# Performance work log

Measured on AMD Instinct MI355X. Metric: run time of the kernel, lower is better.

Reference implementation:

```python
import jax, jax.numpy as jnp
import numpy as np

INPUT_SIZE = 256
HIDDEN_SIZE = 512


def setup_inputs() -> dict:
    key = jax.random.key(0)
    ks = jax.random.split(key, 14)
    B, L, I, H = 64, 1024, INPUT_SIZE, HIDDEN_SIZE
    s = (1.0 / H) ** 0.5
    u = lambda k, shape: jax.random.uniform(k, shape, jnp.float32, -s, s)
    return {
        "inputs": jax.random.normal(ks[0], (B, L, I), jnp.float32),
        "hidden_states": jnp.zeros((1, B, H), jnp.float32),
        "w_ir": u(ks[1], (H, I)), "w_iz": u(ks[2], (H, I)), "w_in": u(ks[3], (H, I)),
        "b_ir": u(ks[4], (H,)), "b_iz": u(ks[5], (H,)), "b_in": u(ks[6], (H,)),
        "w_hr": u(ks[7], (H, H)), "w_hz": u(ks[8], (H, H)), "w_hn": u(ks[9], (H, H)),
        "b_hr": u(ks[10], (H,)), "b_hz": u(ks[11], (H,)), "b_hn": u(ks[12], (H,)),
    }


def _gru(inputs, h0, w_ir, w_iz, w_in, b_ir, b_iz, b_in,
         w_hr, w_hz, w_hn, b_hr, b_hz, b_hn):
    # Precompute all input projections in one big GEMM each (same math as per-step).
    # shapes: inputs [B,L,I] -> [B,L,H]
    xr = jnp.einsum("bli,hi->blh", inputs, w_ir) + b_ir
    xz = jnp.einsum("bli,hi->blh", inputs, w_iz) + b_iz
    xn = jnp.einsum("bli,hi->blh", inputs, w_in) + b_in

    def step(h, xt):
        xr_t, xz_t, xn_t = xt  # each [B,H]
        r = jax.nn.sigmoid(xr_t + h @ w_hr.T + b_hr)
        z = jax.nn.sigmoid(xz_t + h @ w_hz.T + b_hz)
        n = jnp.tanh(xn_t + r * (h @ w_hn.T + b_hn))
        h_new = (1.0 - z) * n + z * h
        return h_new, h_new

    # scan over time: move L to leading axis
    xs = (xr.transpose(1, 0, 2), xz.transpose(1, 0, 2), xn.transpose(1, 0, 2))
    h_last, hs = jax.lax.scan(step, h0[0], xs)  # hs: [L,B,H]
    outputs = hs.transpose(1, 0, 2)  # [B,L,H]
    return outputs, h_last[None]  # final hidden kept as (1,B,H) like the torch module


def reference(inputs, hidden_states, w_ir, w_iz, w_in, b_ir, b_iz, b_in,
              w_hr, w_hz, w_hn, b_hr, b_hz, b_hn):
    return _gru(inputs, hidden_states, w_ir, w_iz, w_in, b_ir, b_iz, b_in,
                w_hr, w_hz, w_hn, b_hr, b_hz, b_hn)
```

## Files before the change

kernel.cpp:

```cpp
#include <hip/hip_runtime.h>
#include <hip/hip_bf16.h>

typedef __attribute__((ext_vector_type(8))) short bf16x8;
typedef __attribute__((ext_vector_type(4))) float f32x4;


__device__ __forceinline__ unsigned short f2bf(float f) {
    __hip_bfloat16 h = __float2bfloat16(f);
    return __builtin_bit_cast(unsigned short, h);
}
__device__ __forceinline__ float bf2f(unsigned short u) {
    union { unsigned int i; float f; } c; c.i = ((unsigned int)u) << 16; return c.f;
}

__device__ __forceinline__ void store_h64(unsigned long long* p, unsigned long long v) {
    asm volatile("global_store_dwordx2 %0, %1, off sc0 sc1" :: "v"(p), "v"(v) : "memory");
}
__device__ __forceinline__ void store_flag(unsigned int* p, unsigned int v) {
    asm volatile("global_store_dword %0, %1, off sc0 sc1" :: "v"(p), "v"(v) : "memory");
}
__device__ __forceinline__ void vmem_drain() {
    asm volatile("s_waitcnt vmcnt(0)" ::: "memory");
}
__device__ __forceinline__ void lds_drain() {
    asm volatile("s_waitcnt lgkmcnt(0)" ::: "memory");
}

__global__ void pack_inputs(const float* __restrict__ in, unsigned short* __restrict__ out) {
    int i = blockIdx.x * 256 + threadIdx.x;
    float4 v = reinterpret_cast<const float4*>(in)[i];
    ushort4 u;
    u.x = f2bf(v.x); u.y = f2bf(v.y); u.z = f2bf(v.z); u.w = f2bf(v.w);
    reinterpret_cast<ushort4*>(out)[i] = u;
}

__global__ void pack_weights(const float* __restrict__ w_ir, const float* __restrict__ w_iz,
                             const float* __restrict__ w_in, const float* __restrict__ b_ir,
                             const float* __restrict__ b_iz, const float* __restrict__ b_in,
                             const float* __restrict__ w_hr, const float* __restrict__ w_hz,
                             const float* __restrict__ w_hn, const float* __restrict__ b_hr,
                             const float* __restrict__ b_hz,
                             unsigned short* __restrict__ Wx, unsigned short* __restrict__ Wh,
                             float* __restrict__ biasx, unsigned int* __restrict__ flags) {
    int i = blockIdx.x * 256 + threadIdx.x;
    {
        int g = i / 262144, rem = i % 262144;
        const float* src = (g == 0) ? w_hr : ((g == 1) ? w_hz : w_hn);
        Wh[i] = f2bf(src[rem]);
    }
    if (i < 393216) {
        int g = i / 131072, rem = i % 131072;
        const float* src = (g == 0) ? w_ir : ((g == 1) ? w_iz : w_in);
        Wx[i] = f2bf(src[rem]);
    }
    if (i < 1536) {
        int g = i / 512, j = i % 512;
        float v = (g == 0) ? (b_ir[j] + b_hr[j]) : ((g == 1) ? (b_iz[j] + b_hz[j]) : b_in[j]);
        biasx[i] = v;
    }
    if (i < 4096) flags[i] = 0u;
}

__global__ __launch_bounds__(256) void xproj_gemm(
    const unsigned short* __restrict__ A,
    const unsigned short* __restrict__ Bw,
    const float* __restrict__ biasx,
    unsigned short* __restrict__ X)
{
    __shared__ __attribute__((aligned(16))) unsigned short Al[64][40];
    __shared__ __attribute__((aligned(16))) unsigned short Bl[64][40];
    const int tid  = threadIdx.x;
    const int m0   = blockIdx.x * 64;
    const int n0   = blockIdx.y * 64;
    const int lane = tid & 63;
    const int wv   = tid >> 6;
    const int quad = lane >> 4;
    const int l16  = lane & 15;
    const int mw   = (wv & 1) * 32;
    const int nw   = (wv >> 1) * 32;
    const int lr   = tid >> 2;
    const int lc   = (tid & 3) * 8;

    f32x4 acc[2][2] = {};

    for (int kb = 0; kb < 8; ++kb) {
        uint4 av = *reinterpret_cast<const uint4*>(A  + (size_t)(m0 + lr) * 256 + kb * 32 + lc);
        uint4 bv = *reinterpret_cast<const uint4*>(Bw + (size_t)(n0 + lr) * 256 + kb * 32 + lc);
        __syncthreads();
        *reinterpret_cast<uint4*>(&Al[lr][lc]) = av;
        *reinterpret_cast<uint4*>(&Bl[lr][lc]) = bv;
        __syncthreads();
        bf16x8 af[2], bfg[2];
#pragma unroll
        for (int s = 0; s < 2; ++s) {
            af[s]  = *reinterpret_cast<const bf16x8*>(&Al[mw + s * 16 + l16][quad * 8]);
            bfg[s] = *reinterpret_cast<const bf16x8*>(&Bl[nw + s * 16 + l16][quad * 8]);
        }
#pragma unroll
        for (int sm = 0; sm < 2; ++sm)
#pragma unroll
            for (int sn = 0; sn < 2; ++sn)
                acc[sm][sn] = __builtin_amdgcn_mfma_f32_16x16x32_bf16(af[sm], bfg[sn], acc[sm][sn], 0, 0, 0);
    }
#pragma unroll
    for (int sn = 0; sn < 2; ++sn) {
        int n = n0 + nw + sn * 16 + l16;
        float bias = biasx[n];
#pragma unroll
        for (int sm = 0; sm < 2; ++sm)
#pragma unroll
            for (int r = 0; r < 4; ++r) {
                int m = m0 + mw + sm * 16 + quad * 4 + r;
                int t = m & 1023, b = m >> 10;
                X[(size_t)(t * 64 + b) * 1536 + n] = f2bf(acc[sm][sn][r] + bias);
            }
    }
}

__global__ __launch_bounds__(512, 1) void gru_scan(
    const unsigned short* __restrict__ X,
    const unsigned short* __restrict__ Wh,
    const float* __restrict__ h0,
    const float* __restrict__ b_hn,
    unsigned long long* __restrict__ Hp64,
    unsigned int* __restrict__ flags,
    float* __restrict__ out)
{
    const int tid  = threadIdx.x;
    const int lane = tid & 63;
    const int wv   = tid >> 6;
    const int mg   = wv & 3;
    const int kh   = wv >> 2;
    const int quad = lane >> 4;
    const int jl   = lane & 15;
    const int bid  = blockIdx.x;
    const int jg   = bid * 16 + jl;

    __shared__ __attribute__((aligned(16))) f32x4 red[2][3][4][64];
    __shared__ __attribute__((aligned(16))) unsigned short tsc[4][256];

    bf16x8 bfrag[3][8];
#pragma unroll
    for (int g = 0; g < 3; ++g)
#pragma unroll
        for (int kk = 0; kk < 8; ++kk) {
            uint4 v = *reinterpret_cast<const uint4*>(
                Wh + (size_t)(g * 512 + jg) * 512 + kh * 256 + kk * 32 + quad * 8);
            bfrag[g][kk] = __builtin_bit_cast(bf16x8, v);
        }
    const float bhn = b_hn[jg];

    unsigned int* const flag_my = flags + (bid * 4 + mg) * 32;
    const unsigned int* const fpoll = flags + ((kh * 16 + jl) * 4 + mg) * 32;

    const int myslot = (lane & 15) * 4 + (lane >> 4);

    float h_reg[4];
    float xv[3][4];
    if (kh == 0) {
#pragma unroll
        for (int r = 0; r < 4; ++r) {
            int b = mg * 16 + quad * 4 + r;
            float h = h0[b * 512 + jg];
            h_reg[r] = h;
            tsc[mg][(quad * 4 + r) * 16 + jl] = f2bf(h);
        }
        lds_drain();
        {
            unsigned long long tv = *reinterpret_cast<const unsigned long long*>(
                &tsc[mg][(lane & 15) * 16 + (lane >> 4) * 4]);
            store_h64(Hp64 + ((size_t)mg * 32 + bid) * 64 + myslot, tv);
        }
        vmem_drain();
        if (lane == 0) store_flag(flag_my, 1u);
#pragma unroll
        for (int r = 0; r < 4; ++r) {
            int b = mg * 16 + quad * 4 + r;
#pragma unroll
            for (int g = 0; g < 3; ++g)
                xv[g][r] = bf2f(X[(size_t)b * 1536 + g * 512 + jg]);
        }
    }

    for (int t = 0; t < 1024; ++t) {
        const int cur = t & 1;
        const unsigned int tgt = (unsigned int)(t + 1);

        {
            unsigned int v;
            do { v = __hip_atomic_load(fpoll, __ATOMIC_RELAXED, __HIP_MEMORY_SCOPE_AGENT); }
            while (!__all((int)(v >= tgt)));
        }

        bf16x8 afrag[8];
        {
            const unsigned long long* bs = Hp64 + ((size_t)cur * 4 + mg) * 32 * 64;
#pragma unroll
            for (int kk = 0; kk < 8; ++kk) {
                const int idx = (kh * 16 + kk * 2 + (quad >> 1)) * 64 + jl * 4 + (quad & 1) * 2;
                unsigned long long lo = __hip_atomic_load(bs + idx,     __ATOMIC_RELAXED, __HIP_MEMORY_SCOPE_AGENT);
                unsigned long long hi = __hip_atomic_load(bs + idx + 1, __ATOMIC_RELAXED, __HIP_MEMORY_SCOPE_AGENT);
                ulonglong2 u; u.x = lo; u.y = hi;
                afrag[kk] = __builtin_bit_cast(bf16x8, u);
            }
        }

        f32x4 acc[3];
#pragma unroll
        for (int g = 0; g < 3; ++g) {
            f32x4 a = {0.f, 0.f, 0.f, 0.f};
#pragma unroll
            for (int kk = 0; kk < 8; ++kk)
                a = __builtin_amdgcn_mfma_f32_16x16x32_bf16(afrag[kk], bfrag[g][kk], a, 0, 0, 0);
            acc[g] = a;
        }

        if (kh == 1) {
#pragma unroll
            for (int g = 0; g < 3; ++g)
                red[cur][g][mg][lane] = acc[g];
        }
        __syncthreads();

        if (kh == 0) {
#pragma unroll
            for (int g = 0; g < 3; ++g)
                acc[g] += red[cur][g][mg][lane];

#pragma unroll
            for (int r = 0; r < 4; ++r) {
                float rv = 1.f / (1.f + __expf(-(xv[0][r] + acc[0][r])));
                float zv = 1.f / (1.f + __expf(-(xv[1][r] + acc[1][r])));
                float na = xv[2][r] + rv * (acc[2][r] + bhn);
                float nv = 1.f - 2.f / (1.f + __expf(2.f * na));
                float h  = (1.f - zv) * nv + zv * h_reg[r];
                h_reg[r] = h;
                tsc[mg][(quad * 4 + r) * 16 + jl] = f2bf(h);
            }
            if (t < 1023) {
                lds_drain();
                unsigned long long tv = *reinterpret_cast<const unsigned long long*>(
                    &tsc[mg][(lane & 15) * 16 + (lane >> 4) * 4]);
                store_h64(Hp64 + (((size_t)((t + 1) & 1) * 4 + mg) * 32 + bid) * 64 + myslot, tv);
                vmem_drain();
                if (lane == 0) store_flag(flag_my, (unsigned int)(t + 2));
            }
#pragma unroll
            for (int r = 0; r < 4; ++r) {
                int b = mg * 16 + quad * 4 + r;
                out[(size_t)b * (1024 * 512) + (size_t)t * 512 + jg] = h_reg[r];
            }
            if (t < 1023) {
                const unsigned short* Xt = X + (size_t)(t + 1) * (64 * 1536);
#pragma unroll
                for (int r = 0; r < 4; ++r) {
                    int b = mg * 16 + quad * 4 + r;
#pragma unroll
                    for (int g = 0; g < 3; ++g)
                        xv[g][r] = bf2f(Xt[b * 1536 + g * 512 + jg]);
                }
            } else {
#pragma unroll
                for (int r = 0; r < 4; ++r) {
                    int b = mg * 16 + quad * 4 + r;
                    out[(size_t)(64 * 1024 * 512) + b * 512 + jg] = h_reg[r];
                }
            }
        }
    }
}

extern "C" void kernel_launch(void* const* d_in, const int* in_sizes, int n_in,
                              void* d_out, int out_size, void* d_ws, size_t ws_size,
                              hipStream_t stream) {
    const float* inputs = (const float*)d_in[0];
    const float* h0     = (const float*)d_in[1];
    const float* w_ir   = (const float*)d_in[2];
    const float* w_iz   = (const float*)d_in[3];
    const float* w_in   = (const float*)d_in[4];
    const float* b_ir   = (const float*)d_in[5];
    const float* b_iz   = (const float*)d_in[6];
    const float* b_in   = (const float*)d_in[7];
    const float* w_hr   = (const float*)d_in[8];
    const float* w_hz   = (const float*)d_in[9];
    const float* w_hn   = (const float*)d_in[10];
    const float* b_hr   = (const float*)d_in[11];
    const float* b_hz   = (const float*)d_in[12];
    const float* b_hn   = (const float*)d_in[13];
    float* out = (float*)d_out;

    char* wsb = (char*)d_ws;
    unsigned short*     X     = (unsigned short*)(wsb);
    unsigned short*     Abf   = (unsigned short*)(wsb + 201326592);
    unsigned short*     Wx    = (unsigned short*)(wsb + 234881024);
    unsigned short*     Wh    = (unsigned short*)(wsb + 235667456);
    float*              biasx = (float*)        (wsb + 237240320);
    unsigned long long* Hp64  = (unsigned long long*)(wsb + 237246464);
    unsigned int*       flags = (unsigned int*) (wsb + 237377536);

    pack_inputs<<<16384, 256, 0, stream>>>(inputs, Abf);
    pack_weights<<<3072, 256, 0, stream>>>(w_ir, w_iz, w_in, b_ir, b_iz, b_in,
                                           w_hr, w_hz, w_hn, b_hr, b_hz, Wx, Wh, biasx, flags);
    xproj_gemm<<<dim3(1024, 24), 256, 0, stream>>>(Abf, Wx, biasx, X);
    gru_scan<<<32, 512, 0, stream>>>(X, Wh, h0, b_hn, Hp64, flags, out);
}
```

Measured before the change: 4.633 ms.

## Embed step tags in hidden-state words to replace flag polling handshake

Each bf16 hidden value is now stored in a 32-bit word whose upper half carries a per-step tag, so consumers can load the data and check its freshness in one pass instead of first polling a flag and then loading. The producer-side vmcnt drain between the data store and the flag store is removed, and the flag is kept only as a fallback wait path. This targets the cross-block synchronisation latency on the serial recurrence, at the cost of doubling the size of the exchanged hidden buffer and adding unpacking work.

```diff
diff --git a/kernel.cpp b/kernel.cpp
--- a/kernel.cpp
+++ b/kernel.cpp
@@ -3,6 +3,7 @@
 
 typedef __attribute__((ext_vector_type(8))) short bf16x8;
 typedef __attribute__((ext_vector_type(4))) float f32x4;
+typedef __attribute__((ext_vector_type(4))) unsigned int u32x4;
 
 
 __device__ __forceinline__ unsigned short f2bf(float f) {
@@ -13,14 +14,11 @@
     union { unsigned int i; float f; } c; c.i = ((unsigned int)u) << 16; return c.f;
 }
 
-__device__ __forceinline__ void store_h64(unsigned long long* p, unsigned long long v) {
-    asm volatile("global_store_dwordx2 %0, %1, off sc0 sc1" :: "v"(p), "v"(v) : "memory");
+__device__ __forceinline__ void store_tile16(u32x4* p, u32x4 v) {
+    asm volatile("global_store_dwordx4 %0, %1, off sc0 sc1" :: "v"(p), "v"(v) : "memory");
 }
 __device__ __forceinline__ void store_flag(unsigned int* p, unsigned int v) {
     asm volatile("global_store_dword %0, %1, off sc0 sc1" :: "v"(p), "v"(v) : "memory");
-}
-__device__ __forceinline__ void vmem_drain() {
-    asm volatile("s_waitcnt vmcnt(0)" ::: "memory");
 }
 __device__ __forceinline__ void lds_drain() {
     asm volatile("s_waitcnt lgkmcnt(0)" ::: "memory");
@@ -41,7 +39,8 @@
                              const float* __restrict__ w_hn, const float* __restrict__ b_hr,
                              const float* __restrict__ b_hz,
                              unsigned short* __restrict__ Wx, unsigned short* __restrict__ Wh,
-                             float* __restrict__ biasx, unsigned int* __restrict__ flags) {
+                             float* __restrict__ biasx, unsigned int* __restrict__ Hp,
+                             unsigned int* __restrict__ flags) {
     int i = blockIdx.x * 256 + threadIdx.x;
     {
         int g = i / 262144, rem = i % 262144;
@@ -58,6 +57,7 @@
         float v = (g == 0) ? (b_ir[j] + b_hr[j]) : ((g == 1) ? (b_iz[j] + b_hz[j]) : b_in[j]);
         biasx[i] = v;
     }
+    if (i < 65536) Hp[i] = 0u;
     if (i < 4096) flags[i] = 0u;
 }
 
@@ -122,7 +122,7 @@
     const unsigned short* __restrict__ Wh,
     const float* __restrict__ h0,
     const float* __restrict__ b_hn,
-    unsigned long long* __restrict__ Hp64,
+    unsigned int* __restrict__ Hp,
     unsigned int* __restrict__ flags,
     float* __restrict__ out)
 {
@@ -137,7 +137,7 @@
     const int jg   = bid * 16 + jl;
 
     __shared__ __attribute__((aligned(16))) f32x4 red[2][3][4][64];
-    __shared__ __attribute__((aligned(16))) unsigned short tsc[4][256];
+    __shared__ __attribute__((aligned(16))) unsigned int tsc[4][256];
 
     bf16x8 bfrag[3][8];
 #pragma unroll
@@ -153,8 +153,6 @@
     unsigned int* const flag_my = flags + (bid * 4 + mg) * 32;
     const unsigned int* const fpoll = flags + ((kh * 16 + jl) * 4 + mg) * 32;
 
-    const int myslot = (lane & 15) * 4 + (lane >> 4);
-
     float h_reg[4];
     float xv[3][4];
     if (kh == 0) {
@@ -163,15 +161,13 @@
             int b = mg * 16 + quad * 4 + r;
             float h = h0[b * 512 + jg];
             h_reg[r] = h;
-            tsc[mg][(quad * 4 + r) * 16 + jl] = f2bf(h);
+            tsc[mg][(quad * 4 + r) * 16 + jl] = (1u << 16) | (unsigned int)f2bf(h);
         }
         lds_drain();
         {
-            unsigned long long tv = *reinterpret_cast<const unsigned long long*>(
-                &tsc[mg][(lane & 15) * 16 + (lane >> 4) * 4]);
-            store_h64(Hp64 + ((size_t)mg * 32 + bid) * 64 + myslot, tv);
-        }
-        vmem_drain();
+            u32x4 tv = *reinterpret_cast<const u32x4*>(&tsc[mg][lane * 4]);
+            store_tile16(reinterpret_cast<u32x4*>(Hp + (size_t)(mg * 32 + bid) * 256 + lane * 4), tv);
+        }
         if (lane == 0) store_flag(flag_my, 1u);
 #pragma unroll
         for (int r = 0; r < 4; ++r) {
@@ -182,27 +178,51 @@
         }
     }
 
+    const unsigned long long* hb = reinterpret_cast<const unsigned long long*>(Hp);
+    const int lbase = mg * 4096 + (kh * 16 + (quad >> 1)) * 128 + jl * 8 + (quad & 1) * 4;
+
     for (int t = 0; t < 1024; ++t) {
         const int cur = t & 1;
-        const unsigned int tgt = (unsigned int)(t + 1);
-
-        {
+        const unsigned int tag  = (unsigned int)((t >> 1) + 1);
+        const unsigned int tag2 = tag | (tag << 16);
+        const unsigned long long* hs = hb + (size_t)cur * 16384 + lbase;
+
+        unsigned long long w[32];
+        auto loadchk = [&]() -> unsigned int {
+            unsigned int e = 0u;
+#pragma unroll
+            for (int kk = 0; kk < 8; ++kk)
+#pragma unroll
+                for (int p = 0; p < 4; ++p) {
+                    unsigned long long ww = __hip_atomic_load(
+                        hs + kk * 256 + p, __ATOMIC_RELAXED, __HIP_MEMORY_SCOPE_AGENT);
+                    w[kk * 4 + p] = ww;
+                    unsigned int hi = ((unsigned int)(ww >> 16) & 0xFFFFu) |
+                                      ((unsigned int)(ww >> 48) << 16);
+                    e |= hi ^ tag2;
+                }
+            return e;
+        };
+        unsigned int err = loadchk();
+        if (!__all(err == 0u)) {
+            const unsigned int tgt = (unsigned int)(t + 1);
             unsigned int v;
             do { v = __hip_atomic_load(fpoll, __ATOMIC_RELAXED, __HIP_MEMORY_SCOPE_AGENT); }
             while (!__all((int)(v >= tgt)));
+            do { err = loadchk(); } while (!__all(err == 0u));
         }
 
         bf16x8 afrag[8];
-        {
-            const unsigned long long* bs = Hp64 + ((size_t)cur * 4 + mg) * 32 * 64;
-#pragma unroll
-            for (int kk = 0; kk < 8; ++kk) {
-                const int idx = (kh * 16 + kk * 2 + (quad >> 1)) * 64 + jl * 4 + (quad & 1) * 2;
-                unsigned long long lo = __hip_atomic_load(bs + idx,     __ATOMIC_RELAXED, __HIP_MEMORY_SCOPE_AGENT);
-                unsigned long long hi = __hip_atomic_load(bs + idx + 1, __ATOMIC_RELAXED, __HIP_MEMORY_SCOPE_AGENT);
-                ulonglong2 u; u.x = lo; u.y = hi;
-                afrag[kk] = __builtin_bit_cast(bf16x8, u);
-            }
+#pragma unroll
+        for (int kk = 0; kk < 8; ++kk) {
+            uint4 u;
+            unsigned long long w0 = w[kk * 4 + 0], w1 = w[kk * 4 + 1];
+            unsigned long long w2 = w[kk * 4 + 2], w3 = w[kk * 4 + 3];
+            u.x = ((unsigned int)w0 & 0xFFFFu) | (((unsigned int)(w0 >> 32)) << 16);
+            u.y = ((unsigned int)w1 & 0xFFFFu) | (((unsigned int)(w1 >> 32)) << 16);
+            u.z = ((unsigned int)w2 & 0xFFFFu) | (((unsigned int)(w2 >> 32)) << 16);
+            u.w = ((unsigned int)w3 & 0xFFFFu) | (((unsigned int)(w3 >> 32)) << 16);
+            afrag[kk] = __builtin_bit_cast(bf16x8, u);
         }
 
         f32x4 acc[3];
@@ -227,6 +247,7 @@
             for (int g = 0; g < 3; ++g)
                 acc[g] += red[cur][g][mg][lane];
 
+            const unsigned int ntag = (unsigned int)((((unsigned int)(t + 1)) >> 1) + 1) << 16;
 #pragma unroll
             for (int r = 0; r < 4; ++r) {
                 float rv = 1.f / (1.f + __expf(-(xv[0][r] + acc[0][r])));
@@ -235,14 +256,13 @@
                 float nv = 1.f - 2.f / (1.f + __expf(2.f * na));
                 float h  = (1.f - zv) * nv + zv * h_reg[r];
                 h_reg[r] = h;
-                tsc[mg][(quad * 4 + r) * 16 + jl] = f2bf(h);
+                tsc[mg][(quad * 4 + r) * 16 + jl] = ntag | (unsigned int)f2bf(h);
             }
             if (t < 1023) {
                 lds_drain();
-                unsigned long long tv = *reinterpret_cast<const unsigned long long*>(
-                    &tsc[mg][(lane & 15) * 16 + (lane >> 4) * 4]);
-                store_h64(Hp64 + (((size_t)((t + 1) & 1) * 4 + mg) * 32 + bid) * 64 + myslot, tv);
-                vmem_drain();
+                u32x4 tv = *reinterpret_cast<const u32x4*>(&tsc[mg][lane * 4]);
+                store_tile16(reinterpret_cast<u32x4*>(
+                    Hp + ((size_t)(((t + 1) & 1) * 4 + mg) * 32 + bid) * 256 + lane * 4), tv);
                 if (lane == 0) store_flag(flag_my, (unsigned int)(t + 2));
             }
 #pragma unroll
@@ -290,17 +310,17 @@
     float* out = (float*)d_out;
 
     char* wsb = (char*)d_ws;
-    unsigned short*     X     = (unsigned short*)(wsb);
-    unsigned short*     Abf   = (unsigned short*)(wsb + 201326592);
-    unsigned short*     Wx    = (unsigned short*)(wsb + 234881024);
-    unsigned short*     Wh    = (unsigned short*)(wsb + 235667456);
-    float*              biasx = (float*)        (wsb + 237240320);
-    unsigned long long* Hp64  = (unsigned long long*)(wsb + 237246464);
-    unsigned int*       flags = (unsigned int*) (wsb + 237377536);
+    unsigned short* X     = (unsigned short*)(wsb);
+    unsigned short* Abf   = (unsigned short*)(wsb + 201326592);
+    unsigned short* Wx    = (unsigned short*)(wsb + 234881024);
+    unsigned short* Wh    = (unsigned short*)(wsb + 235667456);
+    float*          biasx = (float*)        (wsb + 237240320);
+    unsigned int*   Hp    = (unsigned int*) (wsb + 237246464);
+    unsigned int*   flags = (unsigned int*) (wsb + 237508608);
 
     pack_inputs<<<16384, 256, 0, stream>>>(inputs, Abf);
     pack_weights<<<3072, 256, 0, stream>>>(w_ir, w_iz, w_in, b_ir, b_iz, b_in,
-                                           w_hr, w_hz, w_hn, b_hr, b_hz, Wx, Wh, biasx, flags);
+                                           w_hr, w_hz, w_hn, b_hr, b_hz, Wx, Wh, biasx, Hp, flags);
     xproj_gemm<<<dim3(1024, 24), 256, 0, stream>>>(Abf, Wx, biasx, X);
-    gru_scan<<<32, 512, 0, stream>>>(X, Wh, h0, b_hn, Hp64, flags, out);
-}
+    gru_scan<<<32, 512, 0, stream>>>(X, Wh, h0, b_hn, Hp, flags, out);
+}
```

New measurement: 10.14 ms. +118.9%, slower.
